# Kernel tuning notes

Measured on AMD Instinct MI355X. Metric: run time of the kernel, lower is better.

Reference implementation:

```python
import jax, jax.numpy as jnp
import numpy as np

B, SEQ, F = 256, 2048, 5
IN1, U1, U2 = SEQ * F, 32, 1
UNFOLDS = 6          # ODE solver unfolds per cell call
ELAPSED = 1.0        # elapsed time per call


def _cell_params(key, n_in, n_u):
    ks = jax.random.split(key, 9)
    U = lambda k, shp, lo, hi: jax.random.uniform(k, shp, jnp.float32, lo, hi)
    return dict(
        input_w=jnp.ones((n_in,), jnp.float32),
        input_b=jnp.zeros((n_in,), jnp.float32),
        smu=U(ks[0], (n_in, n_u), 0.3, 0.8),
        ssig=U(ks[1], (n_in, n_u), 3.0, 8.0),
        sW=U(ks[2], (n_in, n_u), 0.001, 1.0),
        serev=2.0 * jax.random.bernoulli(ks[3], 0.5, (n_in, n_u)).astype(jnp.float32) - 1.0,
        mu=U(ks[4], (n_u, n_u), 0.3, 0.8),
        sig=U(ks[5], (n_u, n_u), 3.0, 8.0),
        W=U(ks[6], (n_u, n_u), 0.001, 1.0),
        erev=2.0 * jax.random.bernoulli(ks[7], 0.5, (n_u, n_u)).astype(jnp.float32) - 1.0,
        gleak=jnp.ones((n_u,), jnp.float32),
        vleak=U(ks[8], (n_u,), -0.2, 0.2),
        cm=0.5 * jnp.ones((n_u,), jnp.float32),
    )


def setup_inputs() -> dict:
    key = jax.random.key(0)
    kx, ka, kb = jax.random.split(key, 3)
    inp = {"x": jax.random.normal(kx, (B, SEQ, F), jnp.float32)}
    for pfx, k, n_in, n_u in (("a_", ka, IN1, U1), ("b_", kb, U1, U2)):
        for name, v in _cell_params(k, n_in, n_u).items():
            inp[pfx + name] = v
    return inp


def _ltc(x, iw, ib, smu, ssig, sW, serev, mu, sig, W, erev, gleak, vleak, cm):
    # x: [B, n_in]; input affine mapping
    x = x * iw + ib
    # sensory synapse activations: [B, n_in, n_u]
    sact = sW * jax.nn.sigmoid((x[:, :, None] - smu) * ssig)
    w_num_s = jnp.einsum('biu,iu->bu', sact, serev)   # reversal-weighted sum
    w_den_s = jnp.sum(sact, axis=1)
    cm_t = cm / (ELAPSED / UNFOLDS)                   # [n_u]
    v0 = jnp.zeros((x.shape[0], cm.shape[0]), x.dtype)

    def body(v, _):
        # recurrent synapses: presyn axis 1, postsyn axis 2 -> [B, n_u, n_u]
        wact = W * jax.nn.sigmoid((v[:, :, None] - mu) * sig)
        num = cm_t * v + gleak * vleak + jnp.einsum('bij,ij->bj', wact, erev) + w_num_s
        den = cm_t + gleak + jnp.sum(wact, axis=1) + w_den_s
        return num / den, None

    v, _ = jax.lax.scan(body, v0, None, length=UNFOLDS)
    return v


def reference(x,
              a_input_w, a_input_b, a_smu, a_ssig, a_sW, a_serev,
              a_mu, a_sig, a_W, a_erev, a_gleak, a_vleak, a_cm,
              b_input_w, b_input_b, b_smu, b_ssig, b_sW, b_serev,
              b_mu, b_sig, b_W, b_erev, b_gleak, b_vleak, b_cm):
    bsz = x.shape[0]
    xb = x.reshape(bsz, -1)  # [B, seq*5]
    h = _ltc(xb, a_input_w, a_input_b, a_smu, a_ssig, a_sW, a_serev,
             a_mu, a_sig, a_W, a_erev, a_gleak, a_vleak, a_cm)     # [B, 32]
    h2 = _ltc(h, b_input_w, b_input_b, b_smu, b_ssig, b_sW, b_serev,
              b_mu, b_sig, b_W, b_erev, b_gleak, b_vleak, b_cm)    # [B, 1]
    return jax.nn.sigmoid(h2).reshape(bsz)
```

## Files before the change

### kernel.cpp

```cpp
#include <hip/hip_runtime.h>

#define BATCH 256
#define IN1   10240
#define NU    32
#define SPLITS 128
#define STRIPE (IN1 / SPLITS)
#define BBLK  16
#define LOG2E 1.4426950408889634f

__global__ __launch_bounds__(256) void ltc_pack(
    const float* __restrict__ iw, const float* __restrict__ ibias,
    const float* __restrict__ smu, const float* __restrict__ ssig,
    const float* __restrict__ sW, const float* __restrict__ serev,
    float4* __restrict__ Ppk)
{
    const int idx = blockIdx.x * 256 + threadIdx.x;
    const int i = idx >> 5;
    const float sg = ssig[idx] * LOG2E;
    const float A  = sg * iw[i];
    const float C  = (smu[idx] - ibias[i]) * sg;
    const float w  = sW[idx];
    Ppk[idx] = make_float4(A, C, w, w * serev[idx]);
}

__global__ __launch_bounds__(256, 4) void ltc_sensory_partial(
    const float* __restrict__ x,
    const float4* __restrict__ Ppk,
    float2* __restrict__ part)
{
    const int tid = threadIdx.x;
    const int u   = tid & 31;
    const int il  = (tid >> 5) & 1;
    const int wv  = tid >> 6;
    const int bt  = blockIdx.x;
    const int s   = blockIdx.y;
    const int i0  = s * STRIPE;
    const int bA  = bt * BBLK + wv * 4 + il;
    const int bB  = bA + 2;

    const float*  xrA = x + (size_t)bA * IN1 + i0;
    const float*  xrB = x + (size_t)bB * IN1 + i0;
    const float4* pb  = Ppk + (size_t)i0 * NU + u;

    float anA = 0.f, adA = 0.f, anB = 0.f, adB = 0.f;

#pragma unroll 2
    for (int k4 = 0; k4 < STRIPE / 4; ++k4) {
        const float4 xa = *(const float4*)(xrA + k4 * 4);
        const float4 xb = *(const float4*)(xrB + k4 * 4);
        const float xaf[4] = {xa.x, xa.y, xa.z, xa.w};
        const float xbf[4] = {xb.x, xb.y, xb.z, xb.w};
#pragma unroll
        for (int t = 0; t < 4; ++t) {
            const float4 p = pb[(size_t)(k4 * 4 + t) * NU];
            {
                const float e = __builtin_amdgcn_exp2f(p.y - xaf[t] * p.x);
                const float r = __builtin_amdgcn_rcpf(1.0f + e);
                adA = fmaf(p.z, r, adA);
                anA = fmaf(p.w, r, anA);
            }
            {
                const float e = __builtin_amdgcn_exp2f(p.y - xbf[t] * p.x);
                const float r = __builtin_amdgcn_rcpf(1.0f + e);
                adB = fmaf(p.z, r, adB);
                anB = fmaf(p.w, r, anB);
            }
        }
    }

    float2* po = part + (size_t)s * BATCH * NU;
    po[(size_t)bA * NU + u] = make_float2(anA, adA);
    po[(size_t)bB * NU + u] = make_float2(anB, adB);
}

__global__ __launch_bounds__(256) void ltc_reduce(
    const float2* __restrict__ part, int nsplit, float2* __restrict__ S)
{
    const int tid = threadIdx.x;
    const int b   = blockIdx.x;
    const int u   = tid & 31;
    const int sl  = tid >> 5;

    __shared__ float sred[8][NU][2];

    float sn = 0.f, sd = 0.f;
#pragma unroll 8
    for (int s = sl; s < nsplit; s += 8) {
        const float2 p = part[((size_t)s * BATCH + b) * NU + u];
        sn += p.x;
        sd += p.y;
    }
    sred[sl][u][0] = sn;
    sred[sl][u][1] = sd;
    __syncthreads();

    if (tid >= 32) return;
    float Sn = 0.f, Sd = 0.f;
#pragma unroll
    for (int s2 = 0; s2 < 8; ++s2) {
        Sn += sred[s2][u][0];
        Sd += sred[s2][u][1];
    }
    S[(size_t)b * NU + u] = make_float2(Sn, Sd);
}

__global__ __launch_bounds__(256) void ltc_unfold(
    const float2* __restrict__ S,
    const float* __restrict__ amu, const float* __restrict__ asig,
    const float* __restrict__ aW,  const float* __restrict__ aerev,
    const float* __restrict__ agleak, const float* __restrict__ avleak,
    const float* __restrict__ acm,
    const float* __restrict__ b_iw, const float* __restrict__ b_ib,
    const float* __restrict__ b_smu, const float* __restrict__ b_ssig,
    const float* __restrict__ b_sW,  const float* __restrict__ b_serev,
    const float* __restrict__ b_mu,  const float* __restrict__ b_sig,
    const float* __restrict__ b_W,   const float* __restrict__ b_erev,
    const float* __restrict__ b_gleak, const float* __restrict__ b_vleak,
    const float* __restrict__ b_cm,
    float* __restrict__ out)
{
    const int tid = threadIdx.x;
    const int u   = tid & 31;
    const int bl  = tid >> 5;
    const int b   = blockIdx.x * 8 + bl;

    __shared__ float pAp[NU*NU], pCp[NU*NU];
    __shared__ float pW[NU*NU],  pWE[NU*NU];

    for (int p = tid; p < NU * NU; p += 256) {
        const float sg = asig[p] * LOG2E;
        pAp[p] = sg;
        pCp[p] = amu[p] * sg;
        const float w = aW[p];
        pW[p]  = w;
        pWE[p] = w * aerev[p];
    }
    __syncthreads();

    const float2 Sv = S[(size_t)b * NU + u];
    const float Sn = Sv.x, Sd = Sv.y;

    const float cmt = acm[u] * 6.0f;
    const float gl  = agleak[u];
    const float gv  = gl * avleak[u];

    float v = 0.f;
    for (int k = 0; k < 6; ++k) {
        float rn = 0.f, rd = 0.f;
#pragma unroll
        for (int j = 0; j < NU; ++j) {
            const float vj = __shfl(v, j, 32);
            const int pi = j * NU + u;
            const float e = __builtin_amdgcn_exp2f(pCp[pi] - vj * pAp[pi]);
            const float r = __builtin_amdgcn_rcpf(1.0f + e);
            rn = fmaf(pWE[pi], r, rn);
            rd = fmaf(pW[pi],  r, rd);
        }
        const float num = cmt * v + gv + rn + Sn;
        const float den = cmt + gl + rd + Sd;
        v = num / den;
    }

    const float x2  = v * b_iw[u] + b_ib[u];
    const float e2  = __builtin_amdgcn_exp2f((b_smu[u] - x2) * b_ssig[u] * LOG2E);
    const float s2v = b_sW[u] * __builtin_amdgcn_rcpf(1.0f + e2);
    float wn = s2v * b_serev[u];
    float wd = s2v;
#pragma unroll
    for (int m = 16; m >= 1; m >>= 1) {
        wn += __shfl_xor(wn, m, 32);
        wd += __shfl_xor(wd, m, 32);
    }

    const float bcmt = b_cm[0] * 6.0f;
    const float bgl  = b_gleak[0];
    const float bgv  = bgl * b_vleak[0];
    const float bmu  = b_mu[0], bsig = b_sig[0], bW = b_W[0], berev = b_erev[0];
    float v2 = 0.f;
#pragma unroll
    for (int k = 0; k < 6; ++k) {
        const float ee = __builtin_amdgcn_exp2f((bmu - v2) * bsig * LOG2E);
        const float ws = bW * __builtin_amdgcn_rcpf(1.0f + ee);
        const float num = bcmt * v2 + bgv + ws * berev + wn;
        const float den = bcmt + bgl + ws + wd;
        v2 = num / den;
    }

    if (u == 0)
        out[b] = 1.0f / (1.0f + __builtin_amdgcn_exp2f(-v2 * LOG2E));
}

extern "C" void kernel_launch(void* const* d_in, const int* in_sizes, int n_in,
                              void* d_out, int out_size, void* d_ws, size_t ws_size,
                              hipStream_t stream) {
    const float* x       = (const float*)d_in[0];
    const float* a_iw    = (const float*)d_in[1];
    const float* a_ib    = (const float*)d_in[2];
    const float* a_smu   = (const float*)d_in[3];
    const float* a_ssig  = (const float*)d_in[4];
    const float* a_sW    = (const float*)d_in[5];
    const float* a_serev = (const float*)d_in[6];
    const float* a_mu    = (const float*)d_in[7];
    const float* a_sig   = (const float*)d_in[8];
    const float* a_W     = (const float*)d_in[9];
    const float* a_erev  = (const float*)d_in[10];
    const float* a_gleak = (const float*)d_in[11];
    const float* a_vleak = (const float*)d_in[12];
    const float* a_cm    = (const float*)d_in[13];
    const float* b_iw    = (const float*)d_in[14];
    const float* b_ib    = (const float*)d_in[15];
    const float* b_smu   = (const float*)d_in[16];
    const float* b_ssig  = (const float*)d_in[17];
    const float* b_sW    = (const float*)d_in[18];
    const float* b_serev = (const float*)d_in[19];
    const float* b_mu    = (const float*)d_in[20];
    const float* b_sig   = (const float*)d_in[21];
    const float* b_W     = (const float*)d_in[22];
    const float* b_erev  = (const float*)d_in[23];
    const float* b_gleak = (const float*)d_in[24];
    const float* b_vleak = (const float*)d_in[25];
    const float* b_cm    = (const float*)d_in[26];
    float* out = (float*)d_out;

    float4* Ppk  = (float4*)d_ws;
    float2* part = (float2*)(Ppk + (size_t)IN1 * NU);
    float2* Sarr = part + (size_t)SPLITS * BATCH * NU;

    ltc_pack<<<(IN1 * NU) / 256, 256, 0, stream>>>(
        a_iw, a_ib, a_smu, a_ssig, a_sW, a_serev, Ppk);

    dim3 g1(BATCH / BBLK, SPLITS);
    ltc_sensory_partial<<<g1, 256, 0, stream>>>(x, Ppk, part);

    ltc_reduce<<<BATCH, 256, 0, stream>>>(part, SPLITS, Sarr);

    ltc_unfold<<<BATCH / 8, 256, 0, stream>>>(
        Sarr,
        a_mu, a_sig, a_W, a_erev, a_gleak, a_vleak, a_cm,
        b_iw, b_ib, b_smu, b_ssig, b_sW, b_serev,
        b_mu, b_sig, b_W, b_erev, b_gleak, b_vleak, b_cm,
        out);
}
```

Baseline: 55.13 us.

## Process four batch rows per thread with register double-buffered loads in sensory kernel

Each thread now handles four batch rows instead of two, so every loaded packed sensory parameter float4 is reused across four rows. The block batch tile grows from 16 to 32, which halves the number of blocks in the x grid dimension. The loop is also restructured into an explicit two-stage register double buffer, so the loads for the next group are issued before the current group is computed, hiding memory latency. In exchange, register use per thread rises, which could lower occupancy, and the grid has fewer blocks.

Measured after the change: 49.56 us. -10.1%, faster.

```diff
diff --git a/kernel.cpp b/kernel.cpp
--- a/kernel.cpp
+++ b/kernel.cpp
@@ -5,7 +5,8 @@
 #define NU    32
 #define SPLITS 128
 #define STRIPE (IN1 / SPLITS)
-#define BBLK  16
+#define BBLK  32
+#define NGRP  (STRIPE / 4)
 #define LOG2E 1.4426950408889634f
 
 __global__ __launch_bounds__(256) void ltc_pack(
@@ -23,6 +24,39 @@
     Ppk[idx] = make_float4(A, C, w, w * serev[idx]);
 }
 
+#define LOAD_GRP(p0,p1,p2,p3,x0,x1,x2,x3,g) do {                          \
+    const float4* _pp = pb + (size_t)(g) * 4 * NU;                        \
+    p0 = _pp[0];  p1 = _pp[NU];  p2 = _pp[2*NU];  p3 = _pp[3*NU];         \
+    const int _o = (g) * 4;                                               \
+    x0 = *(const float4*)(xr0 + _o);                                      \
+    x1 = *(const float4*)(xr1 + _o);                                      \
+    x2 = *(const float4*)(xr2 + _o);                                      \
+    x3 = *(const float4*)(xr3 + _o);                                      \
+} while (0)
+
+#define SIG4(p, v0, v1, v2, v3) do {                                      \
+    float e, r;                                                           \
+    e = __builtin_amdgcn_exp2f(p.y - (v0) * p.x);                         \
+    r = __builtin_amdgcn_rcpf(1.0f + e);                                  \
+    ad0 = fmaf(p.z, r, ad0); an0 = fmaf(p.w, r, an0);                     \
+    e = __builtin_amdgcn_exp2f(p.y - (v1) * p.x);                         \
+    r = __builtin_amdgcn_rcpf(1.0f + e);                                  \
+    ad1 = fmaf(p.z, r, ad1); an1 = fmaf(p.w, r, an1);                     \
+    e = __builtin_amdgcn_exp2f(p.y - (v2) * p.x);                         \
+    r = __builtin_amdgcn_rcpf(1.0f + e);                                  \
+    ad2 = fmaf(p.z, r, ad2); an2 = fmaf(p.w, r, an2);                     \
+    e = __builtin_amdgcn_exp2f(p.y - (v3) * p.x);                         \
+    r = __builtin_amdgcn_rcpf(1.0f + e);                                  \
+    ad3 = fmaf(p.z, r, ad3); an3 = fmaf(p.w, r, an3);                     \
+} while (0)
+
+#define COMP_GRP(p0,p1,p2,p3,x0,x1,x2,x3) do {                            \
+    SIG4(p0, x0.x, x1.x, x2.x, x3.x);                                     \
+    SIG4(p1, x0.y, x1.y, x2.y, x3.y);                                     \
+    SIG4(p2, x0.z, x1.z, x2.z, x3.z);                                     \
+    SIG4(p3, x0.w, x1.w, x2.w, x3.w);                                     \
+} while (0)
+
 __global__ __launch_bounds__(256, 4) void ltc_sensory_partial(
     const float* __restrict__ x,
     const float4* __restrict__ Ppk,
@@ -35,42 +69,37 @@
     const int bt  = blockIdx.x;
     const int s   = blockIdx.y;
     const int i0  = s * STRIPE;
-    const int bA  = bt * BBLK + wv * 4 + il;
-    const int bB  = bA + 2;
-
-    const float*  xrA = x + (size_t)bA * IN1 + i0;
-    const float*  xrB = x + (size_t)bB * IN1 + i0;
-    const float4* pb  = Ppk + (size_t)i0 * NU + u;
-
-    float anA = 0.f, adA = 0.f, anB = 0.f, adB = 0.f;
-
-#pragma unroll 2
-    for (int k4 = 0; k4 < STRIPE / 4; ++k4) {
-        const float4 xa = *(const float4*)(xrA + k4 * 4);
-        const float4 xb = *(const float4*)(xrB + k4 * 4);
-        const float xaf[4] = {xa.x, xa.y, xa.z, xa.w};
-        const float xbf[4] = {xb.x, xb.y, xb.z, xb.w};
-#pragma unroll
-        for (int t = 0; t < 4; ++t) {
-            const float4 p = pb[(size_t)(k4 * 4 + t) * NU];
-            {
-                const float e = __builtin_amdgcn_exp2f(p.y - xaf[t] * p.x);
-                const float r = __builtin_amdgcn_rcpf(1.0f + e);
-                adA = fmaf(p.z, r, adA);
-                anA = fmaf(p.w, r, anA);
-            }
-            {
-                const float e = __builtin_amdgcn_exp2f(p.y - xbf[t] * p.x);
-                const float r = __builtin_amdgcn_rcpf(1.0f + e);
-                adB = fmaf(p.z, r, adB);
-                anB = fmaf(p.w, r, anB);
-            }
-        }
-    }
+    const int b0  = bt * BBLK + wv * 8 + il * 4;
+
+    const float* xr0 = x + (size_t)(b0 + 0) * IN1 + i0;
+    const float* xr1 = x + (size_t)(b0 + 1) * IN1 + i0;
+    const float* xr2 = x + (size_t)(b0 + 2) * IN1 + i0;
+    const float* xr3 = x + (size_t)(b0 + 3) * IN1 + i0;
+    const float4* pb = Ppk + (size_t)i0 * NU + u;
+
+    float an0 = 0.f, ad0 = 0.f, an1 = 0.f, ad1 = 0.f;
+    float an2 = 0.f, ad2 = 0.f, an3 = 0.f, ad3 = 0.f;
+
+    float4 pA0, pA1, pA2, pA3, xA0, xA1, xA2, xA3;
+    float4 pB0, pB1, pB2, pB3, xB0, xB1, xB2, xB3;
+
+    LOAD_GRP(pA0,pA1,pA2,pA3, xA0,xA1,xA2,xA3, 0);
+#pragma unroll 1
+    for (int g = 0; g < NGRP - 2; g += 2) {
+        LOAD_GRP(pB0,pB1,pB2,pB3, xB0,xB1,xB2,xB3, g + 1);
+        COMP_GRP(pA0,pA1,pA2,pA3, xA0,xA1,xA2,xA3);
+        LOAD_GRP(pA0,pA1,pA2,pA3, xA0,xA1,xA2,xA3, g + 2);
+        COMP_GRP(pB0,pB1,pB2,pB3, xB0,xB1,xB2,xB3);
+    }
+    LOAD_GRP(pB0,pB1,pB2,pB3, xB0,xB1,xB2,xB3, NGRP - 1);
+    COMP_GRP(pA0,pA1,pA2,pA3, xA0,xA1,xA2,xA3);
+    COMP_GRP(pB0,pB1,pB2,pB3, xB0,xB1,xB2,xB3);
 
     float2* po = part + (size_t)s * BATCH * NU;
-    po[(size_t)bA * NU + u] = make_float2(anA, adA);
-    po[(size_t)bB * NU + u] = make_float2(anB, adB);
+    po[(size_t)(b0 + 0) * NU + u] = make_float2(an0, ad0);
+    po[(size_t)(b0 + 1) * NU + u] = make_float2(an1, ad1);
+    po[(size_t)(b0 + 2) * NU + u] = make_float2(an2, ad2);
+    po[(size_t)(b0 + 3) * NU + u] = make_float2(an3, ad3);
 }
 
 __global__ __launch_bounds__(256) void ltc_reduce(
```

## Stage x tile in shared memory and reuse each parameter across sixteen batches

Applied to the files above, without the earlier changes.

The sensory partial kernel now loads a 64-batch by 40-input slice of x into shared memory, transposed, and each thread keeps 16 batch accumulators. Each packed parameter float4 is loaded once and reused across those 16 batches, where before it served only 2. The two half-waves split the input index by parity and are combined with a cross-lane shuffle. Splits double to 256 and the batch block grows to 64, which gives more partials for the reduce kernel to read and higher register pressure from the 32 accumulators per thread.

After: 49.24 us. 1.12x faster.

```diff
diff --git a/kernel.cpp b/kernel.cpp
--- a/kernel.cpp
+++ b/kernel.cpp
@@ -3,9 +3,10 @@
 #define BATCH 256
 #define IN1   10240
 #define NU    32
-#define SPLITS 128
+#define SPLITS 256
 #define STRIPE (IN1 / SPLITS)
-#define BBLK  16
+#define NPAIR  (STRIPE / 2)
+#define BBLK  64
 #define LOG2E 1.4426950408889634f
 
 __global__ __launch_bounds__(256) void ltc_pack(
@@ -23,54 +24,87 @@
     Ppk[idx] = make_float4(A, C, w, w * serev[idx]);
 }
 
+#define SIGQ(q, base) do {                                                \
+    float e_, r_;                                                         \
+    e_ = __builtin_amdgcn_exp2f(p.y - (q).x * p.x);                       \
+    r_ = __builtin_amdgcn_rcpf(1.0f + e_);                                \
+    ad[(base)+0] = fmaf(p.z, r_, ad[(base)+0]);                           \
+    an[(base)+0] = fmaf(p.w, r_, an[(base)+0]);                           \
+    e_ = __builtin_amdgcn_exp2f(p.y - (q).y * p.x);                       \
+    r_ = __builtin_amdgcn_rcpf(1.0f + e_);                                \
+    ad[(base)+1] = fmaf(p.z, r_, ad[(base)+1]);                           \
+    an[(base)+1] = fmaf(p.w, r_, an[(base)+1]);                           \
+    e_ = __builtin_amdgcn_exp2f(p.y - (q).z * p.x);                       \
+    r_ = __builtin_amdgcn_rcpf(1.0f + e_);                                \
+    ad[(base)+2] = fmaf(p.z, r_, ad[(base)+2]);                           \
+    an[(base)+2] = fmaf(p.w, r_, an[(base)+2]);                           \
+    e_ = __builtin_amdgcn_exp2f(p.y - (q).w * p.x);                       \
+    r_ = __builtin_amdgcn_rcpf(1.0f + e_);                                \
+    ad[(base)+3] = fmaf(p.z, r_, ad[(base)+3]);                           \
+    an[(base)+3] = fmaf(p.w, r_, an[(base)+3]);                           \
+} while (0)
+
 __global__ __launch_bounds__(256, 4) void ltc_sensory_partial(
     const float* __restrict__ x,
     const float4* __restrict__ Ppk,
     float2* __restrict__ part)
 {
-    const int tid = threadIdx.x;
-    const int u   = tid & 31;
-    const int il  = (tid >> 5) & 1;
-    const int wv  = tid >> 6;
-    const int bt  = blockIdx.x;
-    const int s   = blockIdx.y;
-    const int i0  = s * STRIPE;
-    const int bA  = bt * BBLK + wv * 4 + il;
-    const int bB  = bA + 2;
-
-    const float*  xrA = x + (size_t)bA * IN1 + i0;
-    const float*  xrB = x + (size_t)bB * IN1 + i0;
-    const float4* pb  = Ppk + (size_t)i0 * NU + u;
-
-    float anA = 0.f, adA = 0.f, anB = 0.f, adB = 0.f;
+    const int tid  = threadIdx.x;
+    const int lane = tid & 63;
+    const int u    = tid & 31;
+    const int bh   = (tid >> 5) & 1;
+    const int w    = tid >> 6;
+    const int bt   = blockIdx.x;
+    const int s    = blockIdx.y;
+    const int b0   = bt * BBLK;
+    const int i0   = s * STRIPE;
+
+    __shared__ float xT[STRIPE][BBLK];
+
+    for (int idx = tid; idx < BBLK * (STRIPE / 4); idx += 256) {
+        const int r  = idx & (BBLK - 1);
+        const int c4 = idx >> 6;
+        const float4 v = *(const float4*)(x + (size_t)(b0 + r) * IN1 + i0 + c4 * 4);
+        xT[c4 * 4 + 0][r] = v.x;
+        xT[c4 * 4 + 1][r] = v.y;
+        xT[c4 * 4 + 2][r] = v.z;
+        xT[c4 * 4 + 3][r] = v.w;
+    }
+    __syncthreads();
+
+    const float4* pb = Ppk + (size_t)i0 * NU + lane;
+
+    float an[16], ad[16];
+#pragma unroll
+    for (int k = 0; k < 16; ++k) { an[k] = 0.f; ad[k] = 0.f; }
 
 #pragma unroll 2
-    for (int k4 = 0; k4 < STRIPE / 4; ++k4) {
-        const float4 xa = *(const float4*)(xrA + k4 * 4);
-        const float4 xb = *(const float4*)(xrB + k4 * 4);
-        const float xaf[4] = {xa.x, xa.y, xa.z, xa.w};
-        const float xbf[4] = {xb.x, xb.y, xb.z, xb.w};
-#pragma unroll
-        for (int t = 0; t < 4; ++t) {
-            const float4 p = pb[(size_t)(k4 * 4 + t) * NU];
-            {
-                const float e = __builtin_amdgcn_exp2f(p.y - xaf[t] * p.x);
-                const float r = __builtin_amdgcn_rcpf(1.0f + e);
-                adA = fmaf(p.z, r, adA);
-                anA = fmaf(p.w, r, anA);
-            }
-            {
-                const float e = __builtin_amdgcn_exp2f(p.y - xbf[t] * p.x);
-                const float r = __builtin_amdgcn_rcpf(1.0f + e);
-                adB = fmaf(p.z, r, adB);
-                anB = fmaf(p.w, r, anB);
-            }
-        }
-    }
-
-    float2* po = part + (size_t)s * BATCH * NU;
-    po[(size_t)bA * NU + u] = make_float2(anA, adA);
-    po[(size_t)bB * NU + u] = make_float2(anB, adB);
+    for (int ip = 0; ip < NPAIR; ++ip) {
+        const float4 p = pb[ip * 64];
+        const int il = ip * 2 + bh;
+        const float4* xrow = (const float4*)&xT[il][w * 16];
+        const float4 q0 = xrow[0];
+        const float4 q1 = xrow[1];
+        const float4 q2 = xrow[2];
+        const float4 q3 = xrow[3];
+        SIGQ(q0, 0);
+        SIGQ(q1, 4);
+        SIGQ(q2, 8);
+        SIGQ(q3, 12);
+    }
+
+#pragma unroll
+    for (int k = 0; k < 16; ++k) {
+        an[k] += __shfl_xor(an[k], 32, 64);
+        ad[k] += __shfl_xor(ad[k], 32, 64);
+    }
+
+    if (bh == 0) {
+        float2* po = part + ((size_t)s * BATCH + b0 + w * 16) * NU + u;
+#pragma unroll
+        for (int k = 0; k < 16; ++k)
+            po[(size_t)k * NU] = make_float2(an[k], ad[k]);
+    }
 }
 
 __global__ __launch_bounds__(256) void ltc_reduce(
```

## Restructure sensory kernel: register-blocked batch, pairwise sigmoid fusion, LDS reduction

Applied to the files above, without the earlier changes.

Each thread now holds parameters for two inputs in registers and loops over 32 batch rows. It combines the two sigmoids over a common denominator, so one reciprocal serves two exponentials. Partial sums across the 8 input lanes per block are reduced with a cross-half-wave shuffle and LDS before being written. This cuts transcendental work and parameter reloads, but adds register pressure from 32 float2 accumulators, strided 8-byte x loads across rows, and a clamp to avoid overflow in the product of denominators.

Result: slower. 160.6 us (+191.2%).

```diff
diff --git a/kernel.cpp b/kernel.cpp
--- a/kernel.cpp
+++ b/kernel.cpp
@@ -3,9 +3,10 @@
 #define BATCH 256
 #define IN1   10240
 #define NU    32
+#define NB    32
+#define BGROUPS (BATCH / NB)
 #define SPLITS 128
 #define STRIPE (IN1 / SPLITS)
-#define BBLK  16
 #define LOG2E 1.4426950408889634f
 
 __global__ __launch_bounds__(256) void ltc_pack(
@@ -30,47 +31,58 @@
 {
     const int tid = threadIdx.x;
     const int u   = tid & 31;
-    const int il  = (tid >> 5) & 1;
-    const int wv  = tid >> 6;
-    const int bt  = blockIdx.x;
-    const int s   = blockIdx.y;
-    const int i0  = s * STRIPE;
-    const int bA  = bt * BBLK + wv * 4 + il;
-    const int bB  = bA + 2;
-
-    const float*  xrA = x + (size_t)bA * IN1 + i0;
-    const float*  xrB = x + (size_t)bB * IN1 + i0;
-    const float4* pb  = Ppk + (size_t)i0 * NU + u;
-
-    float anA = 0.f, adA = 0.f, anB = 0.f, adB = 0.f;
-
-#pragma unroll 2
-    for (int k4 = 0; k4 < STRIPE / 4; ++k4) {
-        const float4 xa = *(const float4*)(xrA + k4 * 4);
-        const float4 xb = *(const float4*)(xrB + k4 * 4);
-        const float xaf[4] = {xa.x, xa.y, xa.z, xa.w};
-        const float xbf[4] = {xb.x, xb.y, xb.z, xb.w};
-#pragma unroll
-        for (int t = 0; t < 4; ++t) {
-            const float4 p = pb[(size_t)(k4 * 4 + t) * NU];
-            {
-                const float e = __builtin_amdgcn_exp2f(p.y - xaf[t] * p.x);
-                const float r = __builtin_amdgcn_rcpf(1.0f + e);
-                adA = fmaf(p.z, r, adA);
-                anA = fmaf(p.w, r, anA);
-            }
-            {
-                const float e = __builtin_amdgcn_exp2f(p.y - xbf[t] * p.x);
-                const float r = __builtin_amdgcn_rcpf(1.0f + e);
-                adB = fmaf(p.z, r, adB);
-                anB = fmaf(p.w, r, anB);
-            }
+    const int il  = tid >> 5;
+    const int w   = tid >> 6;
+    const int b0  = blockIdx.x * NB;
+    const int i0  = blockIdx.y * STRIPE;
+
+    float2 acc[NB];
+#pragma unroll
+    for (int n = 0; n < NB; ++n) acc[n] = make_float2(0.f, 0.f);
+
+    for (int rnd = 0; rnd < STRIPE / 16; ++rnd) {
+        const int pi = i0 + (rnd * 8 + il) * 2;
+        const float4 P0 = Ppk[(size_t)pi * NU + u];
+        const float4 P1 = Ppk[(size_t)(pi + 1) * NU + u];
+        const float w01  = P0.z + P1.z;
+        const float we01 = P0.w + P1.w;
+        const float* xp = x + pi;
+#pragma unroll
+        for (int n = 0; n < NB; ++n) {
+            const float2 xv = *(const float2*)(xp + (size_t)(b0 + n) * IN1);
+            const float t0 = fminf(30.f, P0.y - xv.x * P0.x);
+            const float t1 = fminf(30.f, P1.y - xv.y * P1.x);
+            const float e0 = __builtin_amdgcn_exp2f(t0);
+            const float e1 = __builtin_amdgcn_exp2f(t1);
+            const float D  = (1.0f + e0) * (1.0f + e1);
+            const float rD = __builtin_amdgcn_rcpf(D);
+            const float numN = fmaf(P1.w, e0, fmaf(P0.w, e1, we01));
+            const float numD = fmaf(P1.z, e0, fmaf(P0.z, e1, w01));
+            acc[n].x = fmaf(numN, rD, acc[n].x);
+            acc[n].y = fmaf(numD, rD, acc[n].y);
         }
     }
 
-    float2* po = part + (size_t)s * BATCH * NU;
-    po[(size_t)bA * NU + u] = make_float2(anA, adA);
-    po[(size_t)bB * NU + u] = make_float2(anB, adB);
+    __shared__ float wred[4][NB][NU][2];
+#pragma unroll
+    for (int n = 0; n < NB; ++n) {
+        const float vn = acc[n].x + __shfl_xor(acc[n].x, 32, 64);
+        const float vd = acc[n].y + __shfl_xor(acc[n].y, 32, 64);
+        if ((tid & 63) < 32) {
+            wred[w][n][u][0] = vn;
+            wred[w][n][u][1] = vd;
+        }
+    }
+    __syncthreads();
+    for (int p = tid; p < NB * NU; p += 256) {
+        const int n = p >> 5, uu = p & 31;
+        const float sn = wred[0][n][uu][0] + wred[1][n][uu][0]
+                       + wred[2][n][uu][0] + wred[3][n][uu][0];
+        const float sd = wred[0][n][uu][1] + wred[1][n][uu][1]
+                       + wred[2][n][uu][1] + wred[3][n][uu][1];
+        part[((size_t)blockIdx.y * BATCH + (b0 + n)) * NU + uu] =
+            make_float2(sn, sd);
+    }
 }
 
 __global__ __launch_bounds__(256) void ltc_reduce(
@@ -229,7 +241,7 @@
     ltc_pack<<<(IN1 * NU) / 256, 256, 0, stream>>>(
         a_iw, a_ib, a_smu, a_ssig, a_sW, a_serev, Ppk);
 
-    dim3 g1(BATCH / BBLK, SPLITS);
+    dim3 g1(BGROUPS, SPLITS);
     ltc_sensory_partial<<<g1, 256, 0, stream>>>(x, Ppk, part);
 
     ltc_reduce<<<BATCH, 256, 0, stream>>>(part, SPLITS, Sarr);
```
